# Performance work log

Hardware: AMD Instinct MI355X
Metric: run time of the kernel (lower is better)

Reference implementation:

```python
import jax, jax.numpy as jnp
import numpy as np

EPS = 1e-6

def _linear_params(key, d_in, d_out):
    w = jax.random.normal(key, (d_in, d_out), dtype=jnp.float32) * np.sqrt(2.0 / (d_in + d_out))
    b = jnp.zeros((d_out,), dtype=jnp.float32)
    return w, b

def setup_inputs() -> dict:
    key = jax.random.key(0)
    ks = jax.random.split(key, 8)
    B, S, D = 4, 2048, 1024
    x = jax.random.normal(ks[0], (B, S, D), dtype=jnp.float32)
    wq, bq = _linear_params(ks[1], D, D)
    wk, bk = _linear_params(ks[2], D, D)
    wv, bv = _linear_params(ks[3], D, D)
    wo, bo = _linear_params(ks[4], D, D)
    w1, b1 = _linear_params(ks[5], D, D)
    w2, b2 = _linear_params(ks[6], D, D)
    g1 = jnp.ones((D,), jnp.float32); be1 = jnp.zeros((D,), jnp.float32)
    g2 = jnp.ones((D,), jnp.float32); be2 = jnp.zeros((D,), jnp.float32)
    return {"x": x, "wq": wq, "bq": bq, "wk": wk, "bk": bk, "wv": wv, "bv": bv,
            "wo": wo, "bo": bo, "w1": w1, "b1": b1, "w2": w2, "b2": b2,
            "g1": g1, "be1": be1, "g2": g2, "be2": be2}

def _layernorm(x, gamma, beta):
    mean = jnp.mean(x, axis=-1, keepdims=True)
    # torch .std() default is unbiased (ddof=1); eps added to std (not var)
    std = jnp.std(x, axis=-1, keepdims=True, ddof=1)
    return gamma * (x - mean) / (std + EPS) + beta

def _attention(x, wq, bq, wk, bk, wv, bv, wo, bo):
    S = x.shape[-2]
    q = x @ wq + bq  # [B,S,D]
    k = x @ wk + bk
    v = x @ wv + bv
    scores = jnp.einsum('bsd,btd->bst', q, k) / jnp.sqrt(jnp.asarray(S, jnp.float32))
    causal = jnp.tril(jnp.ones((S, S), dtype=bool))  # keep lower triangle incl. diag
    scores = jnp.where(causal, scores, -jnp.inf)
    attn = jax.nn.softmax(scores, axis=-1)
    out = jnp.einsum('bst,btd->bsd', attn, v)
    return out @ wo + bo

def reference(x, wq, bq, wk, bk, wv, bv, wo, bo, w1, b1, w2, b2, g1, be1, g2, be2):
    h = _attention(_layernorm(x, g1, be1), wq, bq, wk, bk, wv, bv, wo, bo) + x
    m = _layernorm(h, g2, be2)
    m = jnp.maximum(m @ w1 + b1, 0.0) @ w2 + b2
    return m + h
```

## Files before the change

kernel.cpp:

```cpp
#include <hip/hip_runtime.h>
#include <math.h>

#define BB 4
#define SS 2048
#define DD 1024
#define MM (BB*SS)
#define SD ((size_t)SS*DD)
#define MD ((size_t)MM*DD)
#define PPB ((size_t)2162688)

#define WT_OFF (3*MD + 4*PPB)
#define ZP_OFF (WT_OFF + 6*(size_t)DD*DD)
#define LF_OFF (ZP_OFF + 16)
#define REQ_WS ((LF_OFF + 16384) * 2)

constexpr float LN_EPS = 1e-6f;

typedef __attribute__((ext_vector_type(8))) __bf16 bf16x8;
typedef __attribute__((ext_vector_type(4))) float f32x4;

__device__ __forceinline__ unsigned short f2bfbits(float f){
    unsigned u = __float_as_uint(f);
    u += 0x7FFFu + ((u >> 16) & 1u);
    return (unsigned short)(u >> 16);
}
__device__ __forceinline__ int rowWidth(int s){ return ((s >> 6) + 1) << 6; }
__device__ __forceinline__ size_t rowOff(int s){
    int g = s >> 6;
    return (size_t)4096 * (size_t)((g * (g + 1)) >> 1) + (size_t)(s & 63) * (size_t)((g + 1) << 6);
}
__device__ __forceinline__ void gl_lds(const unsigned short* g, unsigned short* l){
    __builtin_amdgcn_global_load_lds(
        (const __attribute__((address_space(1))) unsigned int*)g,
        (__attribute__((address_space(3))) unsigned int*)l, 16, 0, 0);
}

__device__ __forceinline__ int3 xcd_swz(){
    const int gx = gridDim.x, gy = gridDim.y, gz = gridDim.z;
    const int n = gx * gy * gz;
    int lin = blockIdx.x + gx * (blockIdx.y + gy * blockIdx.z);
    const int cpx = n >> 3;
    lin = (lin & 7) * cpx + (lin >> 3);
    int3 r;
    r.x = lin % gx; lin /= gx;
    r.y = lin % gy;
    r.z = lin / gy;
    return r;
}

__global__ __launch_bounds__(256)
void sentinel_kernel(float* __restrict__ out, const float val){
    out[(size_t)blockIdx.x * 256 + threadIdx.x] = val;
}

struct WPack { const float* w[6]; unsigned short* o[6]; unsigned short* zp; float* lf; };
struct PrepArgs { WPack wp; const float* x; const float* g1; const float* be1;
                  unsigned short* ln; };
__global__ __launch_bounds__(256)
void prep(PrepArgs pa)
{
    const int id = blockIdx.x;
    const int tid = threadIdx.x;
    if (id < 1536){
        __shared__ float Ts[64][65];
        const int z = id >> 8, rem = id & 255;
        const int yy = rem >> 4, xx = rem & 15;
        const float* W = pa.wp.w[z];
        unsigned short* WT = pa.wp.o[z];
        const int r0 = yy*64, c0 = xx*64;
        if (id == 0 && tid < 16) pa.wp.zp[tid] = 0;
        if (id < 16){
            float2 z2 = {0.f, 0.f};
            ((float2*)pa.wp.lf)[id*256 + tid] = z2;
        }
        #pragma unroll
        for (int i = 0; i < 16; ++i){
            int lin = tid + i*256;
            int r = lin >> 6, c = lin & 63;
            Ts[r][c] = W[(size_t)(r0+r)*DD + c0+c];
        }
        __syncthreads();
        #pragma unroll
        for (int i = 0; i < 16; ++i){
            int lin = tid + i*256;
            int r = lin >> 6, c = lin & 63;
            WT[(size_t)(c0+r)*DD + r0+c] = f2bfbits(Ts[c][r]);
        }
    } else {
        __shared__ float red[4];
        const int row = id - 1536;
        float4 xv = ((const float4*)(pa.x + (size_t)row*DD))[tid];
        float v[4] = {xv.x, xv.y, xv.z, xv.w};
        float s = v[0]+v[1]+v[2]+v[3];
        #pragma unroll
        for (int off = 32; off > 0; off >>= 1) s += __shfl_down(s, off, 64);
        if ((tid & 63) == 0) red[tid >> 6] = s;
        __syncthreads();
        const float mean = (red[0]+red[1]+red[2]+red[3]) * (1.0f/DD);
        __syncthreads();
        float q = 0.f;
        #pragma unroll
        for (int i = 0; i < 4; ++i){ float d = v[i]-mean; q += d*d; }
        #pragma unroll
        for (int off = 32; off > 0; off >>= 1) q += __shfl_down(q, off, 64);
        if ((tid & 63) == 0) red[tid >> 6] = q;
        __syncthreads();
        const float var = (red[0]+red[1]+red[2]+red[3]) * (1.0f/(DD-1));
        const float inv = 1.0f/(sqrtf(var) + LN_EPS);
        float4 g4 = ((const float4*)pa.g1)[tid];
        float4 b4 = ((const float4*)pa.be1)[tid];
        ushort4 o;
        o.x = f2bfbits(g4.x*(v[0]-mean)*inv + b4.x);
        o.y = f2bfbits(g4.y*(v[1]-mean)*inv + b4.y);
        o.z = f2bfbits(g4.z*(v[2]-mean)*inv + b4.z);
        o.w = f2bfbits(g4.w*(v[3]-mean)*inv + b4.w);
        ((ushort4*)(pa.ln + (size_t)row*DD))[tid] = o;
    }
}

__global__ __launch_bounds__(256)
void ln_f32(const float* __restrict__ x, const float* __restrict__ gamma,
            const float* __restrict__ beta, unsigned short* __restrict__ out)
{
    __shared__ float red[4];
    const int row = blockIdx.x;
    const int tid = threadIdx.x;
    float4 xv = ((const float4*)(x + (size_t)row*DD))[tid];
    float v[4] = {xv.x, xv.y, xv.z, xv.w};
    float s = v[0]+v[1]+v[2]+v[3];
    #pragma unroll
    for (int off = 32; off > 0; off >>= 1) s += __shfl_down(s, off, 64);
    if ((tid & 63) == 0) red[tid >> 6] = s;
    __syncthreads();
    const float mean = (red[0]+red[1]+red[2]+red[3]) * (1.0f/DD);
    __syncthreads();
    float q = 0.f;
    #pragma unroll
    for (int i = 0; i < 4; ++i){ float d = v[i]-mean; q += d*d; }
    #pragma unroll
    for (int off = 32; off > 0; off >>= 1) q += __shfl_down(q, off, 64);
    if ((tid & 63) == 0) red[tid >> 6] = q;
    __syncthreads();
    const float var = (red[0]+red[1]+red[2]+red[3]) * (1.0f/(DD-1));
    const float inv = 1.0f/(sqrtf(var) + LN_EPS);
    float4 g4 = ((const float4*)gamma)[tid];
    float4 b4 = ((const float4*)beta)[tid];
    ushort4 o;
    o.x = f2bfbits(g4.x*(v[0]-mean)*inv + b4.x);
    o.y = f2bfbits(g4.y*(v[1]-mean)*inv + b4.y);
    o.z = f2bfbits(g4.z*(v[2]-mean)*inv + b4.z);
    o.w = f2bfbits(g4.w*(v[3]-mean)*inv + b4.w);
    ((ushort4*)(out + (size_t)row*DD))[tid] = o;
}

template<bool PACKED>
__device__ __forceinline__ void mfma_db(
    const unsigned short* const ga[4], const unsigned short* const gb[4],
    const int* pw, const unsigned short* zpad, const int NT,
    f32x4 acc[4][4], const int wave, const int lane,
    unsigned short (&As0)[8192], unsigned short (&Bs0)[8192],
    unsigned short (&As1)[8192], unsigned short (&Bs1)[8192])
{
    const int quad = lane >> 4, l15 = lane & 15;
    const int wm = ((wave >> 1) & 1) * 64, wn = (wave & 1) * 64;

    auto stage = [&](unsigned short (&Ab)[8192], unsigned short (&Bb)[8192], const int koff){
        #pragma unroll
        for (int c = 0; c < 4; ++c){
            const unsigned short* gp = ga[c] + koff;
            if constexpr (PACKED) { if (koff >= pw[c]) gp = zpad; }
            gl_lds(gp, &Ab[(wave*4+c)*512]);
            gl_lds(gb[c] + koff, &Bb[(wave*4+c)*512]);
        }
    };
    auto compute = [&](unsigned short (&Ab)[8192], unsigned short (&Bb)[8192]){
        #pragma unroll
        for (int kk = 0; kk < 2; ++kk){
            bf16x8 af[4], bfr[4];
            #pragma unroll
            for (int t = 0; t < 4; ++t){
                const int ra = wm + t*16 + l15, rb = wn + t*16 + l15, gi = kk*4 + quad;
                af[t]  = *(const bf16x8*)&Ab[ra*64 + (((gi + ra) & 7) << 3)];
                bfr[t] = *(const bf16x8*)&Bb[rb*64 + (((gi + rb) & 7) << 3)];
            }
            #pragma unroll
            for (int i = 0; i < 4; ++i)
                #pragma unroll
                for (int j = 0; j < 4; ++j)
                    acc[i][j] = __builtin_amdgcn_mfma_f32_16x16x32_bf16(af[i], bfr[j], acc[i][j], 0, 0, 0);
        }
    };

    stage(As0, Bs0, 0);
    const int half = NT >> 1;
    for (int i = 0; i < half; ++i){
        stage(As1, Bs1, (2*i + 1) << 6);
        asm volatile("s_waitcnt vmcnt(8)" ::: "memory");
        __builtin_amdgcn_s_barrier();
        __builtin_amdgcn_sched_barrier(0);
        compute(As0, Bs0);
        __builtin_amdgcn_s_barrier();
        if (i + 1 < half){
            stage(As0, Bs0, (2*i + 2) << 6);
            asm volatile("s_waitcnt vmcnt(8)" ::: "memory");
        } else {
            asm volatile("s_waitcnt vmcnt(0)" ::: "memory");
        }
        __builtin_amdgcn_s_barrier();
        __builtin_amdgcn_sched_barrier(0);
        compute(As1, Bs1);
        __builtin_amdgcn_s_barrier();
    }
}

__device__ __forceinline__ void mk_chunks(const unsigned short* base, size_t ld, int r0,
                                          int wave, int lane, const unsigned short* g[4]){
    #pragma unroll
    for (int c = 0; c < 4; ++c){
        const int mr = (wave*4 + c)*8 + (lane >> 3);
        const int gk = ((lane & 7) - mr) & 7;
        g[c] = base + (size_t)(r0 + mr)*ld + gk*8;
    }
}

#define DECL_DB \
    __shared__ unsigned short As0[8192]; \
    __shared__ unsigned short Bs0[8192]; \
    __shared__ unsigned short As1[8192]; \
    __shared__ unsigned short Bs1[8192];

template<bool RELU, bool RES, bool OUTF, bool BIAS_M>
__device__ __forceinline__ void gemm_core(
    const unsigned short* __restrict__ A, const unsigned short* __restrict__ B,
    const float* __restrict__ bias, const float* __restrict__ resF,
    unsigned short* __restrict__ outB, float* __restrict__ outF,
    const int N, const int K, const int lda, const int ldb,
    const int m0, const int n0,
    unsigned short (&As0)[8192], unsigned short (&Bs0)[8192],
    unsigned short (&As1)[8192], unsigned short (&Bs1)[8192])
{
    const int tid = threadIdx.x, lane = tid & 63, wave = tid >> 6;
    const int wm = ((wave >> 1) & 1) * 64, wn = (wave & 1) * 64;
    const int quad = lane >> 4, l15 = lane & 15;
    const unsigned short* ga[4]; const unsigned short* gb[4];
    mk_chunks(A, lda, m0, wave, lane, ga);
    mk_chunks(B, ldb, n0, wave, lane, gb);
    f32x4 acc[4][4] = {};
    mfma_db<false>(ga, gb, nullptr, nullptr, K >> 6, acc, wave, lane, As0, Bs0, As1, Bs1);
    #pragma unroll
    for (int i = 0; i < 4; ++i){
        #pragma unroll
        for (int r = 0; r < 4; ++r){
            const int m = m0 + wm + i*16 + quad*4 + r;
            const float bm = BIAS_M ? bias[m] : 0.f;
            #pragma unroll
            for (int j = 0; j < 4; ++j){
                const int n = n0 + wn + j*16 + l15;
                float v = acc[i][j][r] + (BIAS_M ? bm : bias[n]);
                if constexpr (RELU) v = fmaxf(v, 0.f);
                if constexpr (RES) v += resF[(size_t)m*N + n];
                if constexpr (OUTF) outF[(size_t)m*N + n] = v;
                else outB[(size_t)m*N + n] = f2bfbits(v);
            }
        }
    }
}

template<bool RELU, bool RES, bool OUTF, bool BIAS_M>
__global__ __launch_bounds__(256)
void gemm_mfma(const unsigned short* __restrict__ A, const unsigned short* __restrict__ B,
               const float* __restrict__ bias, const float* __restrict__ resF,
               unsigned short* __restrict__ outB, float* __restrict__ outF,
               const int N, const int K, const int lda, const int ldb)
{
    DECL_DB
    const int3 b = xcd_swz();
    gemm_core<RELU,RES,OUTF,BIAS_M>(A, B, bias, resF, outB, outF, N, K, lda, ldb,
                                    b.y*128, b.x*128, As0, Bs0, As1, Bs1);
}

__global__ __launch_bounds__(256)
void proj_fused(const unsigned short* __restrict__ LN,
                const unsigned short* __restrict__ WqT, const unsigned short* __restrict__ WkT,
                const unsigned short* __restrict__ WvT,
                const float* __restrict__ bq, const float* __restrict__ bk,
                const float* __restrict__ bv,
                unsigned short* __restrict__ Qw, unsigned short* __restrict__ Kw,
                unsigned short* __restrict__ VTw)
{
    DECL_DB
    const int lin = blockIdx.x;
    const int id = (lin & 7) * 192 + (lin >> 3);
    if (id < 1024){
        const bool isK = (id >= 512);
        const int q = id & 511;
        const int n0 = (q & 7) * 128, m0 = (q >> 3) * 128;
        gemm_core<false,false,false,false>(LN, isK ? WkT : WqT, isK ? bk : bq, nullptr,
                                           isK ? Kw : Qw, nullptr, DD, DD, DD, DD,
                                           m0, n0, As0, Bs0, As1, Bs1);
    } else {
        const int q = id - 1024;
        const int m0 = (q & 7) * 128, n0 = (q >> 3) * 128;
        gemm_core<false,false,false,true>(WvT, LN, bv, nullptr, VTw, nullptr,
                                          MM, DD, DD, DD, m0, n0, As0, Bs0, As1, Bs1);
    }
}

__global__ __launch_bounds__(256)
void scores_mfma(const unsigned short* __restrict__ Qb, const unsigned short* __restrict__ Kb,
                 unsigned short* __restrict__ Pb, float* __restrict__ Lf, const float scale)
{
    const int lin = blockIdx.x;
    const int id = (lin & 7) * 68 + (lin >> 3);
    const int z = id / 136;
    const int idx = id - z * 136;
    int y = (int)((sqrtf(8.f * (float)idx + 1.f) - 1.f) * 0.5f);
    while ((y + 1) * (y + 2) / 2 <= idx) ++y;
    while (y * (y + 1) / 2 > idx) --y;
    const int x = idx - y * (y + 1) / 2;
    const int s0 = y * 128, t0 = x * 128;

    const unsigned short* Q  = Qb + (size_t)z*SD;
    const unsigned short* Km = Kb + (size_t)z*SD;
    unsigned short* P        = Pb + (size_t)z*PPB;
    float* L                 = Lf + (size_t)z*SS;
    DECL_DB
    const int tid = threadIdx.x, lane = tid & 63, wave = tid >> 6;
    const int wm = ((wave >> 1) & 1) * 64, wn = (wave & 1) * 64;
    const int quad = lane >> 4, l15 = lane & 15;
    const unsigned short* ga[4]; const unsigned short* gb[4];
    mk_chunks(Q,  DD, s0, wave, lane, ga);
    mk_chunks(Km, DD, t0, wave, lane, gb);
    f32x4 acc[4][4] = {};
    mfma_db<false>(ga, gb, nullptr, nullptr, DD >> 6, acc, wave, lane, As0, Bs0, As1, Bs1);

    #pragma unroll
    for (int i = 0; i < 4; ++i){
        #pragma unroll
        for (int r = 0; r < 4; ++r){
            const int s = s0 + wm + i*16 + quad*4 + r;
            const int width = rowWidth(s);
            unsigned short* pr = P + rowOff(s);
            float psum = 0.f;
            if (t0 + wn < width){
                #pragma unroll
                for (int j = 0; j < 4; ++j){
                    const int t = t0 + wn + j*16 + l15;
                    const float e = (t <= s) ? __expf(acc[i][j][r] * scale) : 0.f;
                    pr[t] = f2bfbits(e);
                    psum += e;
                }
                #pragma unroll
                for (int off = 8; off > 0; off >>= 1) psum += __shfl_xor(psum, off, 64);
                if (l15 == 0) atomicAdd(&L[s], psum);
            }
        }
    }
}

__global__ __launch_bounds__(256)
void pv_mfma(const unsigned short* __restrict__ Pb, const unsigned short* __restrict__ VT,
             unsigned short* __restrict__ Cb, const unsigned short* __restrict__ zpad,
             const float* __restrict__ Lf)
{
    const int yr = blockIdx.y;
    const int y  = (blockIdx.z >= 2) ? (15 - yr) : yr;
    const int s0 = y*128, n0 = blockIdx.x*128;
    const unsigned short* P = Pb + (size_t)blockIdx.z*PPB;
    unsigned short* C       = Cb + (size_t)blockIdx.z*SD;
    const float* L          = Lf + (size_t)blockIdx.z*SS;
    const int bcol = blockIdx.z*SS;
    DECL_DB
    const int tid = threadIdx.x, lane = tid & 63, wave = tid >> 6;
    const int wm = ((wave >> 1) & 1) * 64, wn = (wave & 1) * 64;
    const int quad = lane >> 4, l15 = lane & 15;
    const unsigned short* ga[4]; const unsigned short* gb[4]; int pw[4];
    #pragma unroll
    for (int c = 0; c < 4; ++c){
        const int mr = (wave*4 + c)*8 + (lane >> 3);
        const int gk = ((lane & 7) - mr) & 7;
        const int s = s0 + mr;
        pw[c] = rowWidth(s) - gk*8;
        ga[c] = P + rowOff(s) + gk*8;
    }
    mk_chunks(VT + bcol, MM, n0, wave, lane, gb);
    f32x4 acc[4][4] = {};
    const int NT = (s0 >> 6) + 2;
    mfma_db<true>(ga, gb, pw, zpad, NT, acc, wave, lane, As0, Bs0, As1, Bs1);

    #pragma unroll
    for (int i = 0; i < 4; ++i){
        #pragma unroll
        for (int r = 0; r < 4; ++r){
            const int s = s0 + wm + i*16 + quad*4 + r;
            const float linv = 1.0f / L[s];
            #pragma unroll
            for (int j = 0; j < 4; ++j){
                const int n = n0 + wn + j*16 + l15;
                C[(size_t)s*DD + n] = f2bfbits(acc[i][j][r] * linv);
            }
        }
    }
}

extern "C" void kernel_launch(void* const* d_in, const int* in_sizes, int n_in,
                              void* d_out, int out_size, void* d_ws, size_t ws_size,
                              hipStream_t stream)
{
    (void)in_sizes; (void)n_in; (void)out_size;
    const float* x   = (const float*)d_in[0];
    const float* bq  = (const float*)d_in[2];
    const float* bk  = (const float*)d_in[4];
    const float* bv  = (const float*)d_in[6];
    const float* bo  = (const float*)d_in[8];
    const float* b1  = (const float*)d_in[10];
    const float* b2  = (const float*)d_in[12];
    const float* g1  = (const float*)d_in[13];
    const float* be1 = (const float*)d_in[14];
    const float* g2  = (const float*)d_in[15];
    const float* be2 = (const float*)d_in[16];
    float* outf = (float*)d_out;

    if (ws_size < (size_t)REQ_WS){
        sentinel_kernel<<<dim3((unsigned)(MD/256)), dim3(256), 0, stream>>>(outf, 1.0e9f);
        return;
    }

    unsigned short* wsb = (unsigned short*)d_ws;
    unsigned short* Qw  = wsb;
    unsigned short* Kw  = wsb + MD;
    unsigned short* VTw = wsb + 2*MD;
    unsigned short* Pw  = wsb + 3*MD;
    unsigned short* WT  = wsb + WT_OFF;
    unsigned short* ZP  = wsb + ZP_OFF;
    float*          Lf  = (float*)(wsb + LF_OFF);
    float*          Hf  = (float*)Kw;
    unsigned short* CTX = Qw;
    unsigned short* MIDw= Pw;
    unsigned short* LN  = (unsigned short*)d_out;

    PrepArgs pa;
    static const int widx[6] = {1,3,5,7,9,11};
    for (int i = 0; i < 6; ++i){
        pa.wp.w[i] = (const float*)d_in[widx[i]];
        pa.wp.o[i] = WT + (size_t)i*DD*DD;
    }
    pa.wp.zp = ZP;
    pa.wp.lf = Lf;
    pa.x = x; pa.g1 = g1; pa.be1 = be1; pa.ln = LN;
    unsigned short* WqT = pa.wp.o[0]; unsigned short* WkT = pa.wp.o[1];
    unsigned short* WvT = pa.wp.o[2]; unsigned short* WoT = pa.wp.o[3];
    unsigned short* W1T = pa.wp.o[4]; unsigned short* W2T = pa.wp.o[5];

    const dim3 blk(256);
    const float scale = 1.0f / sqrtf((float)SS);
    const dim3 gA(DD/128, MM/128);

    prep<<<dim3(1536 + MM), blk, 0, stream>>>(pa);
    proj_fused<<<dim3(1536), blk, 0, stream>>>(LN, WqT, WkT, WvT, bq, bk, bv, Qw, Kw, VTw);
    scores_mfma<<<dim3(544), blk, 0, stream>>>(Qw, Kw, Pw, Lf, scale);
    pv_mfma<<<dim3(DD/128, SS/128, BB), blk, 0, stream>>>(Pw, VTw, CTX, ZP, Lf);
    gemm_mfma<false,true,true,false><<<gA, blk, 0, stream>>>(CTX, WoT, bo, x, nullptr, Hf, DD, DD, DD, DD);
    ln_f32<<<dim3(MM), blk, 0, stream>>>(Hf, g2, be2, LN);
    gemm_mfma<true,false,false,false><<<gA, blk, 0, stream>>>(LN, W1T, b1, nullptr, MIDw, nullptr, DD, DD, DD, DD);
    gemm_mfma<false,true,true,false><<<gA, blk, 0, stream>>>(MIDw, W2T, b2, Hf, nullptr, outf, DD, DD, DD, DD);
}
```

Baseline: 333.4 us.

## Replace dense GEMMs with 8-wave 256x128 triple-buffered MFMA kernel

```diff
diff --git a/kernel.cpp b/kernel.cpp
--- a/kernel.cpp
+++ b/kernel.cpp
@@ -33,19 +33,6 @@
     __builtin_amdgcn_global_load_lds(
         (const __attribute__((address_space(1))) unsigned int*)g,
         (__attribute__((address_space(3))) unsigned int*)l, 16, 0, 0);
-}
-
-__device__ __forceinline__ int3 xcd_swz(){
-    const int gx = gridDim.x, gy = gridDim.y, gz = gridDim.z;
-    const int n = gx * gy * gz;
-    int lin = blockIdx.x + gx * (blockIdx.y + gy * blockIdx.z);
-    const int cpx = n >> 3;
-    lin = (lin & 7) * cpx + (lin >> 3);
-    int3 r;
-    r.x = lin % gx; lin /= gx;
-    r.y = lin % gy;
-    r.z = lin / gy;
-    return r;
 }
 
 __global__ __launch_bounds__(256)
@@ -151,6 +138,185 @@
     o.z = f2bfbits(g4.z*(v[2]-mean)*inv + b4.z);
     o.w = f2bfbits(g4.w*(v[3]-mean)*inv + b4.w);
     ((ushort4*)(out + (size_t)row*DD))[tid] = o;
+}
+
+__device__ __forceinline__ void mk8a(const unsigned short* base, size_t ld, int r0,
+                                     int wave, int lane, const unsigned short* g[4]){
+    #pragma unroll
+    for (int c = 0; c < 4; ++c){
+        const int mr = (c*8 + wave)*8 + (lane >> 3);
+        const int gk = ((lane & 7) - mr) & 7;
+        g[c] = base + (size_t)(r0 + mr)*ld + gk*8;
+    }
+}
+__device__ __forceinline__ void mk8b(const unsigned short* base, size_t ld, int r0,
+                                     int wave, int lane, const unsigned short* g[2]){
+    #pragma unroll
+    for (int c = 0; c < 2; ++c){
+        const int mr = (c*8 + wave)*8 + (lane >> 3);
+        const int gk = ((lane & 7) - mr) & 7;
+        g[c] = base + (size_t)(r0 + mr)*ld + gk*8;
+    }
+}
+
+template<bool STAGE, bool WAIT0>
+__device__ __forceinline__ void t_step(
+    const unsigned short* const ga[4], const unsigned short* const gb[2], const int kS,
+    f32x4 (&acc)[4][4], const int wave, const int lane,
+    unsigned short (&RA)[16384], unsigned short (&RB)[8192],
+    unsigned short (&SA)[16384], unsigned short (&SB)[8192])
+{
+    const int quad = lane >> 4, l15 = lane & 15;
+    const int wm = (wave >> 1) * 64;
+    const int wn = (wave & 1) * 64;
+    #pragma unroll
+    for (int kk = 0; kk < 2; ++kk){
+        bf16x8 af[4], bf[4];
+        #pragma unroll
+        for (int f = 0; f < 4; ++f){
+            const int ra = wm + f*16 + l15, rb = wn + f*16 + l15, gi = kk*4 + quad;
+            af[f] = *(const bf16x8*)&RA[ra*64 + (((gi + ra) & 7) << 3)];
+            bf[f] = *(const bf16x8*)&RB[rb*64 + (((gi + rb) & 7) << 3)];
+        }
+        if constexpr (STAGE){
+            if (kk == 0){
+                gl_lds(ga[0] + kS, &SA[(0*8 + wave)*512]);
+                gl_lds(ga[1] + kS, &SA[(1*8 + wave)*512]);
+                gl_lds(ga[2] + kS, &SA[(2*8 + wave)*512]);
+            } else {
+                gl_lds(ga[3] + kS, &SA[(3*8 + wave)*512]);
+                gl_lds(gb[0] + kS, &SB[(0*8 + wave)*512]);
+                gl_lds(gb[1] + kS, &SB[(1*8 + wave)*512]);
+            }
+        }
+        __builtin_amdgcn_s_barrier();
+        asm volatile("s_waitcnt lgkmcnt(0)" ::: "memory");
+        __builtin_amdgcn_sched_barrier(0);
+        __builtin_amdgcn_s_setprio(1);
+        #pragma unroll
+        for (int i = 0; i < 4; ++i)
+            #pragma unroll
+            for (int j = 0; j < 4; ++j)
+                acc[i][j] = __builtin_amdgcn_mfma_f32_16x16x32_bf16(af[i], bf[j], acc[i][j], 0, 0, 0);
+        __builtin_amdgcn_s_setprio(0);
+        if (kk == 1){
+            if constexpr (WAIT0) asm volatile("s_waitcnt vmcnt(0)" ::: "memory");
+            else                 asm volatile("s_waitcnt vmcnt(6)" ::: "memory");
+        }
+        __builtin_amdgcn_s_barrier();
+    }
+}
+
+#define DECL_TRI \
+    __shared__ unsigned short A0[16384]; __shared__ unsigned short B0[8192]; \
+    __shared__ unsigned short A1[16384]; __shared__ unsigned short B1[8192]; \
+    __shared__ unsigned short A2[16384]; __shared__ unsigned short B2[8192];
+
+template<bool RELU, bool RES, bool OUTF, bool BIAS_M>
+__device__ __forceinline__ void gemm8_core(
+    const unsigned short* __restrict__ A, const unsigned short* __restrict__ B,
+    const float* __restrict__ bias, const float* __restrict__ resF,
+    unsigned short* __restrict__ outB, float* __restrict__ outF,
+    const int N, const int lda, const int ldb, const int m0, const int n0,
+    unsigned short (&A0)[16384], unsigned short (&B0)[8192],
+    unsigned short (&A1)[16384], unsigned short (&B1)[8192],
+    unsigned short (&A2)[16384], unsigned short (&B2)[8192])
+{
+    const int tid = threadIdx.x, lane = tid & 63, wave = tid >> 6;
+    const unsigned short* ga[4]; const unsigned short* gb[2];
+    mk8a(A, lda, m0, wave, lane, ga);
+    mk8b(B, ldb, n0, wave, lane, gb);
+    f32x4 acc[4][4] = {};
+
+    #pragma unroll
+    for (int c = 0; c < 4; ++c) gl_lds(ga[c],      &A0[(c*8 + wave)*512]);
+    #pragma unroll
+    for (int c = 0; c < 2; ++c) gl_lds(gb[c],      &B0[(c*8 + wave)*512]);
+    #pragma unroll
+    for (int c = 0; c < 4; ++c) gl_lds(ga[c] + 64, &A1[(c*8 + wave)*512]);
+    #pragma unroll
+    for (int c = 0; c < 2; ++c) gl_lds(gb[c] + 64, &B1[(c*8 + wave)*512]);
+    asm volatile("s_waitcnt vmcnt(6)" ::: "memory");
+    __builtin_amdgcn_s_barrier();
+
+    t_step<true ,false>(ga, gb, 128, acc, wave, lane, A0,B0, A2,B2);
+    t_step<true ,false>(ga, gb, 192, acc, wave, lane, A1,B1, A0,B0);
+    t_step<true ,false>(ga, gb, 256, acc, wave, lane, A2,B2, A1,B1);
+    t_step<true ,false>(ga, gb, 320, acc, wave, lane, A0,B0, A2,B2);
+    t_step<true ,false>(ga, gb, 384, acc, wave, lane, A1,B1, A0,B0);
+    t_step<true ,false>(ga, gb, 448, acc, wave, lane, A2,B2, A1,B1);
+    t_step<true ,false>(ga, gb, 512, acc, wave, lane, A0,B0, A2,B2);
+    t_step<true ,false>(ga, gb, 576, acc, wave, lane, A1,B1, A0,B0);
+    t_step<true ,false>(ga, gb, 640, acc, wave, lane, A2,B2, A1,B1);
+    t_step<true ,false>(ga, gb, 704, acc, wave, lane, A0,B0, A2,B2);
+    t_step<true ,false>(ga, gb, 768, acc, wave, lane, A1,B1, A0,B0);
+    t_step<true ,false>(ga, gb, 832, acc, wave, lane, A2,B2, A1,B1);
+    t_step<true ,false>(ga, gb, 896, acc, wave, lane, A0,B0, A2,B2);
+    t_step<true ,false>(ga, gb, 960, acc, wave, lane, A1,B1, A0,B0);
+    t_step<false,true >(ga, gb, 0,   acc, wave, lane, A2,B2, A2,B2);
+    t_step<false,true >(ga, gb, 0,   acc, wave, lane, A0,B0, A0,B0);
+
+    const int quad = lane >> 4, l15 = lane & 15;
+    const int wm = (wave >> 1) * 64, wn = (wave & 1) * 64;
+    #pragma unroll
+    for (int i = 0; i < 4; ++i){
+        #pragma unroll
+        for (int r = 0; r < 4; ++r){
+            const int m = m0 + wm + i*16 + quad*4 + r;
+            const float bm = BIAS_M ? bias[m] : 0.f;
+            #pragma unroll
+            for (int j = 0; j < 4; ++j){
+                const int n = n0 + wn + j*16 + l15;
+                float v = acc[i][j][r] + (BIAS_M ? bm : bias[n]);
+                if constexpr (RELU) v = fmaxf(v, 0.f);
+                if constexpr (RES) v += resF[(size_t)m*N + n];
+                if constexpr (OUTF) outF[(size_t)m*N + n] = v;
+                else outB[(size_t)m*N + n] = f2bfbits(v);
+            }
+        }
+    }
+}
+
+template<bool RELU, bool RES, bool OUTF, bool BIAS_M>
+__global__ __launch_bounds__(512)
+void gemm8(const unsigned short* __restrict__ A, const unsigned short* __restrict__ B,
+           const float* __restrict__ bias, const float* __restrict__ resF,
+           unsigned short* __restrict__ outB, float* __restrict__ outF,
+           const int N, const int lda, const int ldb)
+{
+    DECL_TRI
+    const int lin = blockIdx.x;
+    const int id = (lin & 7) * 32 + (lin >> 3);
+    const int m0 = (id >> 3) * 256, n0 = (id & 7) * 128;
+    gemm8_core<RELU,RES,OUTF,BIAS_M>(A, B, bias, resF, outB, outF, N, lda, ldb,
+                                     m0, n0, A0,B0,A1,B1,A2,B2);
+}
+
+__global__ __launch_bounds__(512)
+void proj8(const unsigned short* __restrict__ LN,
+           const unsigned short* __restrict__ WqT, const unsigned short* __restrict__ WkT,
+           const unsigned short* __restrict__ WvT,
+           const float* __restrict__ bq, const float* __restrict__ bk,
+           const float* __restrict__ bv,
+           unsigned short* __restrict__ Qw, unsigned short* __restrict__ Kw,
+           unsigned short* __restrict__ VTw)
+{
+    DECL_TRI
+    const int lin = blockIdx.x;
+    const int id = (lin & 7) * 96 + (lin >> 3);
+    if (id < 512){
+        const bool isK = (id >= 256);
+        const int q = id & 255;
+        const int n0 = (q & 7) * 128, m0 = (q >> 3) * 256;
+        gemm8_core<false,false,false,false>(LN, isK ? WkT : WqT, isK ? bk : bq, nullptr,
+                                            isK ? Kw : Qw, nullptr, DD, DD, DD,
+                                            m0, n0, A0,B0,A1,B1,A2,B2);
+    } else {
+        const int v = id - 512;
+        const int m0 = (v & 3) * 256, n0 = (v >> 2) * 128;
+        gemm8_core<false,false,false,true>(WvT, LN, bv, nullptr, VTw, nullptr,
+                                           MM, DD, DD, m0, n0, A0,B0,A1,B1,A2,B2);
+    }
 }
 
 template<bool PACKED>
@@ -228,83 +394,6 @@
     __shared__ unsigned short Bs0[8192]; \
     __shared__ unsigned short As1[8192]; \
     __shared__ unsigned short Bs1[8192];
-
-template<bool RELU, bool RES, bool OUTF, bool BIAS_M>
-__device__ __forceinline__ void gemm_core(
-    const unsigned short* __restrict__ A, const unsigned short* __restrict__ B,
-    const float* __restrict__ bias, const float* __restrict__ resF,
-    unsigned short* __restrict__ outB, float* __restrict__ outF,
-    const int N, const int K, const int lda, const int ldb,
-    const int m0, const int n0,
-    unsigned short (&As0)[8192], unsigned short (&Bs0)[8192],
-    unsigned short (&As1)[8192], unsigned short (&Bs1)[8192])
-{
-    const int tid = threadIdx.x, lane = tid & 63, wave = tid >> 6;
-    const int wm = ((wave >> 1) & 1) * 64, wn = (wave & 1) * 64;
-    const int quad = lane >> 4, l15 = lane & 15;
-    const unsigned short* ga[4]; const unsigned short* gb[4];
-    mk_chunks(A, lda, m0, wave, lane, ga);
-    mk_chunks(B, ldb, n0, wave, lane, gb);
-    f32x4 acc[4][4] = {};
-    mfma_db<false>(ga, gb, nullptr, nullptr, K >> 6, acc, wave, lane, As0, Bs0, As1, Bs1);
-    #pragma unroll
-    for (int i = 0; i < 4; ++i){
-        #pragma unroll
-        for (int r = 0; r < 4; ++r){
-            const int m = m0 + wm + i*16 + quad*4 + r;
-            const float bm = BIAS_M ? bias[m] : 0.f;
-            #pragma unroll
-            for (int j = 0; j < 4; ++j){
-                const int n = n0 + wn + j*16 + l15;
-                float v = acc[i][j][r] + (BIAS_M ? bm : bias[n]);
-                if constexpr (RELU) v = fmaxf(v, 0.f);
-                if constexpr (RES) v += resF[(size_t)m*N + n];
-                if constexpr (OUTF) outF[(size_t)m*N + n] = v;
-                else outB[(size_t)m*N + n] = f2bfbits(v);
-            }
-        }
-    }
-}
-
-template<bool RELU, bool RES, bool OUTF, bool BIAS_M>
-__global__ __launch_bounds__(256)
-void gemm_mfma(const unsigned short* __restrict__ A, const unsigned short* __restrict__ B,
-               const float* __restrict__ bias, const float* __restrict__ resF,
-               unsigned short* __restrict__ outB, float* __restrict__ outF,
-               const int N, const int K, const int lda, const int ldb)
-{
-    DECL_DB
-    const int3 b = xcd_swz();
-    gemm_core<RELU,RES,OUTF,BIAS_M>(A, B, bias, resF, outB, outF, N, K, lda, ldb,
-                                    b.y*128, b.x*128, As0, Bs0, As1, Bs1);
-}
-
-__global__ __launch_bounds__(256)
-void proj_fused(const unsigned short* __restrict__ LN,
-                const unsigned short* __restrict__ WqT, const unsigned short* __restrict__ WkT,
-                const unsigned short* __restrict__ WvT,
-                const float* __restrict__ bq, const float* __restrict__ bk,
-                const float* __restrict__ bv,
-                unsigned short* __restrict__ Qw, unsigned short* __restrict__ Kw,
-                unsigned short* __restrict__ VTw)
-{
-    DECL_DB
-    const int lin = blockIdx.x;
-    const int id = (lin & 7) * 192 + (lin >> 3);
-    if (id < 1024){
-        const bool isK = (id >= 512);
-        const int q = id & 511;
-        const int n0 = (q & 7) * 128, m0 = (q >> 3) * 128;
-        gemm_core<false,false,false,false>(LN, isK ? WkT : WqT, isK ? bk : bq, nullptr,
-                                           isK ? Kw : Qw, nullptr, DD, DD, DD, DD,
-                                           m0, n0, As0, Bs0, As1, Bs1);
-    } else {
-        const int q = id - 1024;
-        const int m0 = (q & 7) * 128, n0 = (q >> 3) * 128;
-        gemm_core<false,false,false,true>(WvT, LN, bv, nullptr, VTw, nullptr,
-                                          MM, DD, DD, DD, m0, n0, As0, Bs0, As1, Bs1);
-    }
-}
 
 __global__ __launch_bounds__(256)
 void scores_mfma(const unsigned short* __restrict__ Qb, const unsigned short* __restrict__ Kb,
@@ -453,15 +542,15 @@
     unsigned short* W1T = pa.wp.o[4]; unsigned short* W2T = pa.wp.o[5];
 
     const dim3 blk(256);
+    const dim3 blk8(512);
     const float scale = 1.0f / sqrtf((float)SS);
-    const dim3 gA(DD/128, MM/128);
 
     prep<<<dim3(1536 + MM), blk, 0, stream>>>(pa);
-    proj_fused<<<dim3(1536), blk, 0, stream>>>(LN, WqT, WkT, WvT, bq, bk, bv, Qw, Kw, VTw);
+    proj8<<<dim3(768), blk8, 0, stream>>>(LN, WqT, WkT, WvT, bq, bk, bv, Qw, Kw, VTw);
     scores_mfma<<<dim3(544), blk, 0, stream>>>(Qw, Kw, Pw, Lf, scale);
     pv_mfma<<<dim3(DD/128, SS/128, BB), blk, 0, stream>>>(Pw, VTw, CTX, ZP, Lf);
-    gemm_mfma<false,true,true,false><<<gA, blk, 0, stream>>>(CTX, WoT, bo, x, nullptr, Hf, DD, DD, DD, DD);
+    gemm8<false,true,true,false><<<dim3(256), blk8, 0, stream>>>(CTX, WoT, bo, x, nullptr, Hf, DD, DD, DD);
     ln_f32<<<dim3(MM), blk, 0, stream>>>(Hf, g2, be2, LN);
-    gemm_mfma<true,false,false,false><<<gA, blk, 0, stream>>>(LN, W1T, b1, nullptr, MIDw, nullptr, DD, DD, DD, DD);
-    gemm_mfma<false,true,true,false><<<gA, blk, 0, stream>>>(MIDw, W2T, b2, Hf, nullptr, outf, DD, DD, DD, DD);
-}
+    gemm8<true,false,false,false><<<dim3(256), blk8, 0, stream>>>(LN, W1T, b1, nullptr, MIDw, nullptr, DD, DD, DD);
+    gemm8<false,true,true,false><<<dim3(256), blk8, 0, stream>>>(MIDw, W2T, b2, Hf, nullptr, outf, DD, DD, DD);
+}
```

Measured after the change: 343.5 us. 1.03x slower.
